# Optimization experiments

Measured on AMD Instinct MI355X. Metric: run time of the kernel, lower is better.

Reference implementation:

```python
import jax, jax.numpy as jnp
import numpy as np

B, S, D = 2, 2048, 2048
H = 16
HD = D // H

def setup_inputs() -> dict:
    key = jax.random.key(0)
    ks = jax.random.split(key, 6)
    s = 1.0 / np.sqrt(D)
    return {
        "inputs": jax.random.normal(ks[0], (B, S, D), dtype=jnp.float32),
        "w_q": jax.random.normal(ks[1], (D, D), dtype=jnp.float32) * s,
        "w_k": jax.random.normal(ks[2], (D, D), dtype=jnp.float32) * s,
        "w_v": jax.random.normal(ks[3], (D, D), dtype=jnp.float32) * s,
        "w_o": jax.random.normal(ks[4], (D, D), dtype=jnp.float32) * s,
        "b_o": jax.random.normal(ks[5], (D,), dtype=jnp.float32) * 0.02,
    }

def reference(inputs, w_q, w_k, w_v, w_o, b_o):
    b, t, _ = inputs.shape
    # Linear layers: y = x @ W^T (weights stored torch-style [out, in])
    q = (inputs @ w_q.T).reshape(b, t, H, HD)
    k = (inputs @ w_k.T).reshape(b, t, H, HD)
    v = (inputs @ w_v.T).reshape(b, t, H, HD)
    # scores: [b, h, t, t]
    scores = jnp.einsum('bqhd,bkhd->bhqk', q, k)
    causal = jnp.triu(jnp.ones((t, t), dtype=bool), k=1)
    scores = jnp.where(causal, -jnp.inf, scores)
    # NOTE: source scales by sqrt(token_num) (keys.shape[2] after transpose), not sqrt(head_dim)
    scale = jnp.float32(t) ** 0.5
    attn = jax.nn.softmax(scores / scale, axis=-1)
    ctx = jnp.einsum('bhqk,bkhd->bqhd', attn, v).reshape(b, t, D)
    return ctx @ w_o.T + b_o
```

## Files before the change

### kernel.cpp

```cpp
#include <hip/hip_runtime.h>


typedef __attribute__((ext_vector_type(8))) short short8;
typedef __attribute__((ext_vector_type(4))) float f32x4;

#define SEQ 2048
#define DM  2048
#define NHD 128
#define NT  32
#define QSCALE (0.022097086912079608f * 1.4426950408889634f)

#define EXP2F(x) __builtin_amdgcn_exp2f(x)
#define WAITV(N) asm volatile("s_waitcnt vmcnt(" #N ")" ::: "memory")

__device__ __forceinline__ unsigned short f2bf(float f) {
  unsigned u = __builtin_bit_cast(unsigned, f);
  u += 0x7FFFu + ((u >> 16) & 1u);
  return (unsigned short)(u >> 16);
}
__device__ __forceinline__ unsigned short f2bf_fast(float f) {
  unsigned u = __builtin_bit_cast(unsigned, f);
  return (unsigned short)((u + 0x8000u) >> 16);
}

__device__ __forceinline__ void gll16(const void* g, void* l) {
  __builtin_amdgcn_global_load_lds((const __attribute__((address_space(1))) void*)g,
                                   (__attribute__((address_space(3))) void*)l, 16, 0, 0);
}

template <int CTRL>
__device__ __forceinline__ float dpp_mv(float x) {
  int xi = __builtin_bit_cast(int, x);
  return __builtin_bit_cast(float,
      __builtin_amdgcn_update_dpp(xi, xi, CTRL, 0xF, 0xF, false));
}
__device__ __forceinline__ float red16_max(float x) {
  x = fmaxf(x, dpp_mv<0xB1>(x));
  x = fmaxf(x, dpp_mv<0x4E>(x));
  x = fmaxf(x, dpp_mv<0x124>(x));
  x = fmaxf(x, dpp_mv<0x128>(x));
  return x;
}
__device__ __forceinline__ float red16_sum(float x) {
  x += dpp_mv<0xB1>(x);
  x += dpp_mv<0x4E>(x);
  x += dpp_mv<0x124>(x);
  x += dpp_mv<0x128>(x);
  return x;
}

__global__ __launch_bounds__(256) void cast_bf16_k(const float* __restrict__ in,
                                                   unsigned short* __restrict__ out,
                                                   int n8) {
  int i = blockIdx.x * 256 + threadIdx.x;
  if (i >= n8) return;
  const f32x4* p = (const f32x4*)in + (size_t)i * 2;
  f32x4 a = p[0], b = p[1];
  short8 o;
  o[0] = (short)f2bf(a[0]); o[1] = (short)f2bf(a[1]);
  o[2] = (short)f2bf(a[2]); o[3] = (short)f2bf(a[3]);
  o[4] = (short)f2bf(b[0]); o[5] = (short)f2bf(b[1]);
  o[6] = (short)f2bf(b[2]); o[7] = (short)f2bf(b[3]);
  *(short8*)(out + (size_t)i * 8) = o;
}

__global__ __launch_bounds__(256) void cast_w4_k(const float* __restrict__ Wq,
                                                 const float* __restrict__ Wk,
                                                 const float* __restrict__ Wv,
                                                 const float* __restrict__ Wo,
                                                 unsigned short* __restrict__ Wqb,
                                                 unsigned short* __restrict__ Wkb,
                                                 unsigned short* __restrict__ Wvb,
                                                 unsigned short* __restrict__ Wob) {
  int i = blockIdx.x * 256 + threadIdx.x;
  int r = i >> 19, j = i & 524287;
  const float* src = (r == 0) ? Wq : (r == 1) ? Wk : (r == 2) ? Wv : Wo;
  unsigned short* dst = (r == 0) ? Wqb : (r == 1) ? Wkb : (r == 2) ? Wvb : Wob;
  float sc = (r == 0) ? QSCALE : 1.0f;
  const f32x4* p = (const f32x4*)src + (size_t)j * 2;
  f32x4 a = p[0], b = p[1];
  short8 o;
  o[0] = (short)f2bf(a[0] * sc); o[1] = (short)f2bf(a[1] * sc);
  o[2] = (short)f2bf(a[2] * sc); o[3] = (short)f2bf(a[3] * sc);
  o[4] = (short)f2bf(b[0] * sc); o[5] = (short)f2bf(b[1] * sc);
  o[6] = (short)f2bf(b[2] * sc); o[7] = (short)f2bf(b[3] * sc);
  *(short8*)(dst + (size_t)j * 8) = o;
}

__device__ __forceinline__ void stage_half(const unsigned short* __restrict__ gbase,
                                           unsigned short* lhalf, int tid) {
#pragma unroll
  for (int c = 0; c < 2; ++c) {
    int G = c * 512 + tid;
    int row = G >> 3, g = G & 7;
    int gs = g ^ (row & 7);
    gll16(gbase + (size_t)row * DM + gs * 8, lhalf + (size_t)G * 8);
  }
}

#define LOADAF(MH)                                                              \
  _Pragma("unroll") for (int mi = 0; mi < 4; ++mi)                              \
    _Pragma("unroll") for (int ks = 0; ks < 2; ++ks) {                          \
      int row = wm * 64 + mi * 16 + lr;                                         \
      af[mi][ks] = *(const short8*)&lA[(MH) * 8192 + row * 64 +                 \
                                       (((ks * 4 + kb) ^ (row & 7)) * 8)];      \
    }

#define PHASE(MH, NH, STG, WV)                                                  \
  {                                                                             \
    const unsigned short* lBh = lB + (NH) * 8192;                               \
    short8 bfr[2][2];                                                           \
    _Pragma("unroll") for (int ni = 0; ni < 2; ++ni)                            \
      _Pragma("unroll") for (int ks = 0; ks < 2; ++ks) {                        \
        int row = wn * 32 + ni * 16 + lr;                                       \
        bfr[ni][ks] = *(const short8*)&lBh[row * 64 + (((ks * 4 + kb) ^ (row & 7)) * 8)]; \
      }                                                                         \
    STG;                                                                        \
    __builtin_amdgcn_s_barrier();                                               \
    __builtin_amdgcn_s_setprio(1);                                              \
    _Pragma("unroll") for (int mi = 0; mi < 4; ++mi)                            \
      _Pragma("unroll") for (int ni = 0; ni < 2; ++ni) {                        \
        acc[MH][NH][mi][ni] = __builtin_amdgcn_mfma_f32_16x16x32_bf16(          \
            af[mi][0], bfr[ni][0], acc[MH][NH][mi][ni], 0, 0, 0);               \
        acc[MH][NH][mi][ni] = __builtin_amdgcn_mfma_f32_16x16x32_bf16(          \
            af[mi][1], bfr[ni][1], acc[MH][NH][mi][ni], 0, 0, 0);               \
      }                                                                         \
    __builtin_amdgcn_s_setprio(0);                                              \
    WV;                                                                         \
    __builtin_amdgcn_s_barrier();                                               \
  }

__device__ __forceinline__ void gemm256_core(const unsigned short* __restrict__ A,
                                             const unsigned short* __restrict__ B,
                                             unsigned short* LA, unsigned short* LB,
                                             f32x4 acc[2][2][4][2], int m0, int n0) {
  const int tid = threadIdx.x;
  const int w = tid >> 6, l = tid & 63;
  const int lr = l & 15, kb = l >> 4;
  const int wm = w >> 2, wn = w & 3;

  stage_half(A + (size_t)m0 * DM, LA, tid);
  stage_half(B + (size_t)n0 * DM, LB, tid);
  stage_half(B + (size_t)n0 * DM + (size_t)128 * DM, LB + 8192, tid);
  stage_half(A + (size_t)m0 * DM + (size_t)128 * DM, LA + 8192, tid);
  WAITV(4);
  __builtin_amdgcn_s_barrier();

#pragma unroll 1
  for (int t = 0; t < NT; ++t) {
    const unsigned short* lA = LA + (t & 1) * 16384;
    const unsigned short* lB = LB + (t & 1) * 16384;
    unsigned short* sA = LA + ((t + 1) & 1) * 16384;
    unsigned short* sB = LB + ((t + 1) & 1) * 16384;
    const unsigned short* gA = A + (size_t)m0 * DM + (t + 1) * 64;
    const unsigned short* gB = B + (size_t)n0 * DM + (t + 1) * 64;
    const bool st = (t + 1 < NT);
    short8 af[4][2];
    LOADAF(0);
    PHASE(0, 0, if (st) stage_half(gA, sA, tid),
                if (st) { WAITV(4); } else { WAITV(2); });
    PHASE(0, 1, if (st) stage_half(gB, sB, tid),
                if (st) { WAITV(4); } else { WAITV(0); });
    LOADAF(1);
    PHASE(1, 0, if (st) stage_half(gB + (size_t)128 * DM, sB + 8192, tid), );
    PHASE(1, 1, if (st) stage_half(gA + (size_t)128 * DM, sA + 8192, tid),
                if (st) { WAITV(4); });
  }
}

__global__ __launch_bounds__(512, 2) void gemm_qk_k(const unsigned short* __restrict__ X,
                                                    const unsigned short* __restrict__ Wq,
                                                    const unsigned short* __restrict__ Wk,
                                                    unsigned short* __restrict__ Qo,
                                                    unsigned short* __restrict__ Ko) {
  __shared__ unsigned short LA[32768];
  __shared__ unsigned short LB[32768];
  const int lin = blockIdx.x + 8 * (blockIdx.y + 16 * blockIdx.z);
  const int c = lin & 7, idx = lin >> 3;
  const int xb = (c & 1) * 4 + ((idx >> 2) & 3);
  const int yb = (c >> 1) * 4 + (idx & 3);
  const int zb = idx >> 4;
  const unsigned short* W = zb ? Wk : Wq;
  unsigned short* Y = zb ? Ko : Qo;
  const int m0 = yb * 256, n0 = xb * 256;
  const int tid = threadIdx.x, w = tid >> 6, l = tid & 63;
  const int lr = l & 15, kb = l >> 4;
  const int wm = w >> 2, wn = w & 3;
  f32x4 acc[2][2][4][2] = {};
  gemm256_core(X, W, LA, LB, acc, m0, n0);
#pragma unroll
  for (int mh = 0; mh < 2; ++mh)
#pragma unroll
    for (int nh = 0; nh < 2; ++nh)
#pragma unroll
      for (int mi = 0; mi < 4; ++mi)
#pragma unroll
        for (int ni = 0; ni < 2; ++ni)
#pragma unroll
          for (int rr = 0; rr < 4; ++rr) {
            int row = m0 + mh * 128 + wm * 64 + mi * 16 + kb * 4 + rr;
            int col = n0 + nh * 128 + wn * 32 + ni * 16 + lr;
            Y[(size_t)row * DM + col] = f2bf(acc[mh][nh][mi][ni][rr]);
          }
}

#define PH2(NH, STG, WV)                                                        \
  {                                                                             \
    const unsigned short* lBh = lB + (NH) * 8192;                               \
    short8 bfr[2][2];                                                           \
    _Pragma("unroll") for (int ni = 0; ni < 2; ++ni)                            \
      _Pragma("unroll") for (int ks = 0; ks < 2; ++ks) {                        \
        int row = wn * 32 + ni * 16 + lr;                                       \
        bfr[ni][ks] = *(const short8*)&lBh[row * 64 + (((ks * 4 + kb) ^ (row & 7)) * 8)]; \
      }                                                                         \
    STG;                                                                        \
    __builtin_amdgcn_s_barrier();                                               \
    __builtin_amdgcn_s_setprio(1);                                              \
    _Pragma("unroll") for (int mi = 0; mi < 4; ++mi)                            \
      _Pragma("unroll") for (int ni = 0; ni < 2; ++ni) {                        \
        acc[NH][mi][ni] = __builtin_amdgcn_mfma_f32_16x16x32_bf16(              \
            af[mi][0], bfr[ni][0], acc[NH][mi][ni], 0, 0, 0);                   \
        acc[NH][mi][ni] = __builtin_amdgcn_mfma_f32_16x16x32_bf16(              \
            af[mi][1], bfr[ni][1], acc[NH][mi][ni], 0, 0, 0);                   \
      }                                                                         \
    __builtin_amdgcn_s_setprio(0);                                              \
    WV;                                                                         \
    __builtin_amdgcn_s_barrier();                                               \
  }

__device__ __forceinline__ void gemm128x256_core(const unsigned short* __restrict__ A,
                                                 const unsigned short* __restrict__ B,
                                                 unsigned short* LA, unsigned short* LB,
                                                 f32x4 acc[2][4][2], int m0, int n0) {
  const int tid = threadIdx.x;
  const int w = tid >> 6, l = tid & 63;
  const int lr = l & 15, kb = l >> 4;
  const int wm = w >> 2, wn = w & 3;

  stage_half(A + (size_t)m0 * DM, LA, tid);
  stage_half(B + (size_t)n0 * DM, LB, tid);
  stage_half(B + (size_t)n0 * DM + (size_t)128 * DM, LB + 8192, tid);
  WAITV(2);
  __builtin_amdgcn_s_barrier();

#pragma unroll 1
  for (int t = 0; t < NT; ++t) {
    const unsigned short* lA = LA + (t & 1) * 8192;
    const unsigned short* lB = LB + (t & 1) * 16384;
    unsigned short* sA = LA + ((t + 1) & 1) * 8192;
    unsigned short* sB = LB + ((t + 1) & 1) * 16384;
    const unsigned short* gA = A + (size_t)m0 * DM + (t + 1) * 64;
    const unsigned short* gB = B + (size_t)n0 * DM + (t + 1) * 64;
    const bool st = (t + 1 < NT);
    short8 af[4][2];
#pragma unroll
    for (int mi = 0; mi < 4; ++mi)
#pragma unroll
      for (int ks = 0; ks < 2; ++ks) {
        int row = wm * 64 + mi * 16 + lr;
        af[mi][ks] = *(const short8*)&lA[row * 64 + (((ks * 4 + kb) ^ (row & 7)) * 8)];
      }
    PH2(0, if (st) stage_half(gA, sA, tid),
           if (st) { WAITV(2); } else { WAITV(0); });
    PH2(1, if (st) { stage_half(gB, sB, tid); stage_half(gB + (size_t)128 * DM, sB + 8192, tid); },
           if (st) { WAITV(2); });
  }
}

__global__ __launch_bounds__(512, 2) void gemm_vt_k(const unsigned short* __restrict__ Wv,
                                                    const unsigned short* __restrict__ X,
                                                    unsigned short* __restrict__ Vt) {
  __shared__ unsigned short LA[16384];
  __shared__ unsigned short LB[32768];
  const int lin = blockIdx.x + 16 * blockIdx.y;
  const int c = lin & 7, idx = lin >> 3;
  const int yb = (c >> 2) * 8 + (idx & 7);
  const int xb = (c & 3) * 4 + (idx >> 3);
  const int m0 = yb * 128, n0 = xb * 256;
  const int tid = threadIdx.x, w = tid >> 6, l = tid & 63;
  const int lr = l & 15, kb = l >> 4;
  const int wm = w >> 2, wn = w & 3;
  f32x4 acc[2][4][2] = {};
  gemm128x256_core(Wv, X, LA, LB, acc, m0, n0);
#pragma unroll
  for (int nh = 0; nh < 2; ++nh)
#pragma unroll
    for (int mi = 0; mi < 4; ++mi)
#pragma unroll
      for (int ni = 0; ni < 2; ++ni)
#pragma unroll
        for (int rr = 0; rr < 4; ++rr) {
          int i = m0 + wm * 64 + mi * 16 + kb * 4 + rr;
          int j = n0 + nh * 128 + wn * 32 + ni * 16 + lr;
          Vt[((size_t)(j >> 11) * 2048 + i) * 2048 + (j & 2047)] = f2bf(acc[nh][mi][ni][rr]);
        }
}

__global__ __launch_bounds__(512, 2) void gemm_o_k(const unsigned short* __restrict__ A,
                                                   const unsigned short* __restrict__ W,
                                                   const float* __restrict__ bias,
                                                   float* __restrict__ Y) {
  __shared__ unsigned short LA[16384];
  __shared__ unsigned short LB[32768];
  const int lin = blockIdx.x + 8 * blockIdx.y;
  const int c = lin & 7, idx = lin >> 3;
  const int yb = (c >> 1) * 8 + (idx & 7);
  const int xb = (c & 1) * 4 + (idx >> 3);
  const int m0 = yb * 128, n0 = xb * 256;
  const int tid = threadIdx.x, w = tid >> 6, l = tid & 63;
  const int lr = l & 15, kb = l >> 4;
  const int wm = w >> 2, wn = w & 3;
  f32x4 acc[2][4][2] = {};
  gemm128x256_core(A, W, LA, LB, acc, m0, n0);
#pragma unroll
  for (int nh = 0; nh < 2; ++nh)
#pragma unroll
    for (int mi = 0; mi < 4; ++mi)
#pragma unroll
      for (int ni = 0; ni < 2; ++ni)
#pragma unroll
        for (int rr = 0; rr < 4; ++rr) {
          int row = m0 + wm * 64 + mi * 16 + kb * 4 + rr;
          int col = n0 + nh * 128 + wn * 32 + ni * 16 + lr;
          Y[(size_t)row * DM + col] = acc[nh][mi][ni][rr] + bias[col];
        }
}

__device__ __forceinline__ void stage_tiles(const unsigned short* __restrict__ Kh,
                                            const unsigned short* __restrict__ Vh,
                                            unsigned short* KL, unsigned short* VL,
                                            int kv0, int t) {
#pragma unroll
  for (int c = 0; c < 4; ++c) {
    int S = c * 256 + t;
    int row = S >> 4, g = (S & 15) ^ (row & 7);
    gll16(Kh + (size_t)(kv0 + row) * DM + g * 8, KL + (size_t)S * 8);
  }
#pragma unroll
  for (int c = 0; c < 4; ++c) {
    int S = c * 256 + t;
    int d = S >> 3, g = (S & 7) ^ (d & 7);
    gll16(Vh + (size_t)d * SEQ + kv0 + g * 8, VL + (size_t)S * 8);
  }
}

__global__ __launch_bounds__(256) void attn_k(const unsigned short* __restrict__ Q,
                                              const unsigned short* __restrict__ K,
                                              const unsigned short* __restrict__ Vt,
                                              unsigned short* __restrict__ O) {
  __shared__ unsigned short KL[2][64 * 128];
  __shared__ unsigned short VL[2][128 * 64];
  __shared__ unsigned short Pb[4][16 * 64];
  const int t = threadIdx.x, w = t >> 6, l = t & 63;
  const int lr = l & 15, kb = l >> 4;
  const int id = blockIdx.x;
  const int xcd = id & 7, slot = id >> 3;
  const int bh = xcd * 4 + (slot & 3);
  const int xpair = slot >> 2;
  const int b = bh >> 4, h = bh & 15;
  const unsigned short* Kh = K + (size_t)b * SEQ * DM + h * NHD;
  const unsigned short* Vh = Vt + (size_t)bh * NHD * SEQ;

#pragma unroll 1
  for (int phase = 0; phase < 2; ++phase) {
    const int xq = phase ? (31 - xpair) : xpair;
    const int q0 = xq * 64;
    const int qw = q0 + w * 16;
    const int nkt = xq + 1;

    short8 qf[4];
    {
      const unsigned short* qp = Q + (size_t)(b * SEQ + qw + lr) * DM + h * NHD + kb * 8;
#pragma unroll
      for (int ks = 0; ks < 4; ++ks) qf[ks] = *(const short8*)(qp + ks * 32);
    }
    f32x4 ctx[8] = {};
    float mrow[4], lrow[4];
#pragma unroll
    for (int r = 0; r < 4; ++r) { mrow[r] = -3.0e4f; lrow[r] = 0.f; }

    stage_tiles(Kh, Vh, KL[0], VL[0], 0, t);
    __syncthreads();

    int cbuf = 0;
#pragma unroll 1
    for (int kt = 0; kt < nkt; ++kt) {
      const int kv0 = kt * 64;
      if (kt + 1 < nkt) stage_tiles(Kh, Vh, KL[cbuf ^ 1], VL[cbuf ^ 1], kv0 + 64, t);
      const unsigned short* Kc = KL[cbuf];
      const unsigned short* Vc = VL[cbuf];
      f32x4 s[4];
#pragma unroll
      for (int ct = 0; ct < 4; ++ct) {
        s[ct] = (f32x4){0.f, 0.f, 0.f, 0.f};
        int krow = ct * 16 + lr;
#pragma unroll
        for (int ks = 0; ks < 4; ++ks) {
          short8 bf = *(const short8*)&Kc[krow * 128 + (((ks * 4 + kb) ^ (krow & 7)) * 8)];
          s[ct] = __builtin_amdgcn_mfma_f32_16x16x32_bf16(qf[ks], bf, s[ct], 0, 0, 0);
        }
      }
      const bool needmask = (kv0 + 63 > qw);
      float pe[4][4];
#pragma unroll
      for (int r = 0; r < 4; ++r) {
        const int qi = qw + kb * 4 + r;
        float mx = -3.0e4f;
#pragma unroll
        for (int ct = 0; ct < 4; ++ct) {
          float v = s[ct][r];
          if (needmask && (kv0 + ct * 16 + lr > qi)) v = -3.0e4f;
          s[ct][r] = v;
          mx = fmaxf(mx, v);
        }
        mx = red16_max(mx);
        if (mx > mrow[r] + 8.f) {
          float alpha = EXP2F(mrow[r] - mx);
          mrow[r] = mx;
          lrow[r] *= alpha;
#pragma unroll
          for (int cc = 0; cc < 8; ++cc) ctx[cc][r] *= alpha;
        }
        float rs = 0.f;
#pragma unroll
        for (int ct = 0; ct < 4; ++ct) {
          float e = EXP2F(s[ct][r] - mrow[r]);
          pe[ct][r] = e;
          rs += e;
        }
        lrow[r] += red16_sum(rs);
      }
#pragma unroll
      for (int ct = 0; ct < 4; ++ct)
#pragma unroll
        for (int r = 0; r < 4; ++r) {
          int prow = kb * 4 + r;
          int g = (ct * 2 + (lr >> 3)) ^ ((prow >> 1) & 7);
          Pb[w][prow * 64 + g * 8 + (lr & 7)] = f2bf_fast(pe[ct][r]);
        }
      short8 pa[2];
#pragma unroll
      for (int ks = 0; ks < 2; ++ks)
        pa[ks] = *(const short8*)&Pb[w][lr * 64 + (((ks * 4 + kb) ^ ((lr >> 1) & 7)) * 8)];
#pragma unroll
      for (int cc = 0; cc < 8; ++cc) {
        int vrow = cc * 16 + lr;
#pragma unroll
        for (int ks = 0; ks < 2; ++ks) {
          short8 vb = *(const short8*)&Vc[vrow * 64 + (((ks * 4 + kb) ^ (vrow & 7)) * 8)];
          ctx[cc] = __builtin_amdgcn_mfma_f32_16x16x32_bf16(pa[ks], vb, ctx[cc], 0, 0, 0);
        }
      }
      __syncthreads();
      cbuf ^= 1;
    }
#pragma unroll
    for (int r = 0; r < 4; ++r) {
      float inv = 1.f / lrow[r];
      size_t rowoff = (size_t)(b * SEQ + qw + kb * 4 + r) * DM + h * NHD;
#pragma unroll
      for (int cc = 0; cc < 8; ++cc)
        O[rowoff + cc * 16 + lr] = f2bf_fast(ctx[cc][r] * inv);
    }
  }
}

extern "C" void kernel_launch(void* const* d_in, const int* in_sizes, int n_in,
                              void* d_out, int out_size, void* d_ws, size_t ws_size,
                              hipStream_t stream) {
  const float* X  = (const float*)d_in[0];
  const float* Wq = (const float*)d_in[1];
  const float* Wk = (const float*)d_in[2];
  const float* Wv = (const float*)d_in[3];
  const float* Wo = (const float*)d_in[4];
  const float* bo = (const float*)d_in[5];
  float* out = (float*)d_out;

  unsigned short* ws = (unsigned short*)d_ws;
  unsigned short* Xb  = ws;
  unsigned short* Wqb = ws + 8388608;
  unsigned short* Wkb = ws + 12582912;
  unsigned short* Wvb = ws + 16777216;
  unsigned short* Wob = ws + 20971520;
  unsigned short* Qb  = ws + 25165824;
  unsigned short* Kb  = ws + 33554432;
  unsigned short* Vtb = ws + 41943040;
  unsigned short* Cb  = ws + 50331648;

  cast_bf16_k<<<4096, 256, 0, stream>>>(X, Xb, 1048576);
  cast_w4_k<<<8192, 256, 0, stream>>>(Wq, Wk, Wv, Wo, Wqb, Wkb, Wvb, Wob);

  gemm_qk_k<<<dim3(8, 16, 2), 512, 0, stream>>>(Xb, Wqb, Wkb, Qb, Kb);
  gemm_vt_k<<<dim3(16, 16), 512, 0, stream>>>(Wvb, Xb, Vtb);
  attn_k<<<512, 256, 0, stream>>>(Qb, Kb, Vtb, Cb);
  gemm_o_k<<<dim3(8, 32), 512, 0, stream>>>(Cb, Wob, bo, out);
}
```

Measured before the change: 252.0 us.

## Share K/V tile loads between paired low and high query blocks in attention

Result: slower. 302.4 us (+20.0%).

```diff
diff --git a/kernel.cpp b/kernel.cpp
--- a/kernel.cpp
+++ b/kernel.cpp
@@ -344,6 +344,76 @@
   }
 }
 
+__device__ __forceinline__ void attn_tile(const unsigned short* __restrict__ Kc,
+                                          const unsigned short* __restrict__ Vc,
+                                          unsigned short* __restrict__ Pw,
+                                          const short8 qf[4], f32x4 ctx[8],
+                                          float mrow[4], float lrow[4],
+                                          int qw, int kv0, int lr, int kb) {
+  f32x4 s[4];
+#pragma unroll
+  for (int ct = 0; ct < 4; ++ct) {
+    s[ct] = (f32x4){0.f, 0.f, 0.f, 0.f};
+    int krow = ct * 16 + lr;
+#pragma unroll
+    for (int ks = 0; ks < 4; ++ks) {
+      short8 bf = *(const short8*)&Kc[krow * 128 + (((ks * 4 + kb) ^ (krow & 7)) * 8)];
+      s[ct] = __builtin_amdgcn_mfma_f32_16x16x32_bf16(qf[ks], bf, s[ct], 0, 0, 0);
+    }
+  }
+  const bool needmask = (kv0 + 63 > qw);
+  float pe[4][4];
+#pragma unroll
+  for (int r = 0; r < 4; ++r) {
+    const int qi = qw + kb * 4 + r;
+    float mx = -3.0e4f;
+#pragma unroll
+    for (int ct = 0; ct < 4; ++ct) {
+      float v = s[ct][r];
+      if (needmask && (kv0 + ct * 16 + lr > qi)) v = -3.0e4f;
+      s[ct][r] = v;
+      mx = fmaxf(mx, v);
+    }
+    mx = red16_max(mx);
+    if (mx > mrow[r] + 8.f) {
+      float alpha = EXP2F(mrow[r] - mx);
+      mrow[r] = mx;
+      lrow[r] *= alpha;
+#pragma unroll
+      for (int cc = 0; cc < 8; ++cc) ctx[cc][r] *= alpha;
+    }
+    float rs = 0.f;
+#pragma unroll
+    for (int ct = 0; ct < 4; ++ct) {
+      float e = EXP2F(s[ct][r] - mrow[r]);
+      pe[ct][r] = e;
+      rs += e;
+    }
+    lrow[r] += red16_sum(rs);
+  }
+#pragma unroll
+  for (int ct = 0; ct < 4; ++ct)
+#pragma unroll
+    for (int r = 0; r < 4; ++r) {
+      int prow = kb * 4 + r;
+      int g = (ct * 2 + (lr >> 3)) ^ ((prow >> 1) & 7);
+      Pw[prow * 64 + g * 8 + (lr & 7)] = f2bf_fast(pe[ct][r]);
+    }
+  short8 pa[2];
+#pragma unroll
+  for (int ks = 0; ks < 2; ++ks)
+    pa[ks] = *(const short8*)&Pw[lr * 64 + (((ks * 4 + kb) ^ ((lr >> 1) & 7)) * 8)];
+#pragma unroll
+  for (int cc = 0; cc < 8; ++cc) {
+    int vrow = cc * 16 + lr;
+#pragma unroll
+    for (int ks = 0; ks < 2; ++ks) {
+      short8 vb = *(const short8*)&Vc[vrow * 64 + (((ks * 4 + kb) ^ (vrow & 7)) * 8)];
+      ctx[cc] = __builtin_amdgcn_mfma_f32_16x16x32_bf16(pa[ks], vb, ctx[cc], 0, 0, 0);
+    }
+  }
+}
+
 __global__ __launch_bounds__(256) void attn_k(const unsigned short* __restrict__ Q,
                                               const unsigned short* __restrict__ K,
                                               const unsigned short* __restrict__ Vt,
@@ -361,106 +431,56 @@
   const unsigned short* Kh = K + (size_t)b * SEQ * DM + h * NHD;
   const unsigned short* Vh = Vt + (size_t)bh * NHD * SEQ;
 
+  const int xqL = xpair, xqH = 31 - xpair;
+  const int qwL = xqL * 64 + w * 16;
+  const int qwH = xqH * 64 + w * 16;
+  const int nkt = xqH + 1;
+
+  short8 qfL[4], qfH[4];
+  {
+    const unsigned short* qpL = Q + (size_t)(b * SEQ + qwL + lr) * DM + h * NHD + kb * 8;
+    const unsigned short* qpH = Q + (size_t)(b * SEQ + qwH + lr) * DM + h * NHD + kb * 8;
+#pragma unroll
+    for (int ks = 0; ks < 4; ++ks) {
+      qfL[ks] = *(const short8*)(qpL + ks * 32);
+      qfH[ks] = *(const short8*)(qpH + ks * 32);
+    }
+  }
+  f32x4 ctxL[8] = {}, ctxH[8] = {};
+  float mL[4], lLs[4], mH[4], lHs[4];
+#pragma unroll
+  for (int r = 0; r < 4; ++r) {
+    mL[r] = -3.0e4f; lLs[r] = 0.f;
+    mH[r] = -3.0e4f; lHs[r] = 0.f;
+  }
+
+  stage_tiles(Kh, Vh, KL[0], VL[0], 0, t);
+  __syncthreads();
+
+  int cbuf = 0;
 #pragma unroll 1
-  for (int phase = 0; phase < 2; ++phase) {
-    const int xq = phase ? (31 - xpair) : xpair;
-    const int q0 = xq * 64;
-    const int qw = q0 + w * 16;
-    const int nkt = xq + 1;
-
-    short8 qf[4];
-    {
-      const unsigned short* qp = Q + (size_t)(b * SEQ + qw + lr) * DM + h * NHD + kb * 8;
-#pragma unroll
-      for (int ks = 0; ks < 4; ++ks) qf[ks] = *(const short8*)(qp + ks * 32);
-    }
-    f32x4 ctx[8] = {};
-    float mrow[4], lrow[4];
-#pragma unroll
-    for (int r = 0; r < 4; ++r) { mrow[r] = -3.0e4f; lrow[r] = 0.f; }
-
-    stage_tiles(Kh, Vh, KL[0], VL[0], 0, t);
+  for (int kt = 0; kt < nkt; ++kt) {
+    const int kv0 = kt * 64;
+    if (kt + 1 < nkt) stage_tiles(Kh, Vh, KL[cbuf ^ 1], VL[cbuf ^ 1], kv0 + 64, t);
+    const unsigned short* Kc = KL[cbuf];
+    const unsigned short* Vc = VL[cbuf];
+    attn_tile(Kc, Vc, Pb[w], qfH, ctxH, mH, lHs, qwH, kv0, lr, kb);
+    if (kt <= xqL)
+      attn_tile(Kc, Vc, Pb[w], qfL, ctxL, mL, lLs, qwL, kv0, lr, kb);
     __syncthreads();
-
-    int cbuf = 0;
-#pragma unroll 1
-    for (int kt = 0; kt < nkt; ++kt) {
-      const int kv0 = kt * 64;
-      if (kt + 1 < nkt) stage_tiles(Kh, Vh, KL[cbuf ^ 1], VL[cbuf ^ 1], kv0 + 64, t);
-      const unsigned short* Kc = KL[cbuf];
-      const unsigned short* Vc = VL[cbuf];
-      f32x4 s[4];
-#pragma unroll
-      for (int ct = 0; ct < 4; ++ct) {
-        s[ct] = (f32x4){0.f, 0.f, 0.f, 0.f};
-        int krow = ct * 16 + lr;
-#pragma unroll
-        for (int ks = 0; ks < 4; ++ks) {
-          short8 bf = *(const short8*)&Kc[krow * 128 + (((ks * 4 + kb) ^ (krow & 7)) * 8)];
-          s[ct] = __builtin_amdgcn_mfma_f32_16x16x32_bf16(qf[ks], bf, s[ct], 0, 0, 0);
-        }
-      }
-      const bool needmask = (kv0 + 63 > qw);
-      float pe[4][4];
-#pragma unroll
-      for (int r = 0; r < 4; ++r) {
-        const int qi = qw + kb * 4 + r;
-        float mx = -3.0e4f;
-#pragma unroll
-        for (int ct = 0; ct < 4; ++ct) {
-          float v = s[ct][r];
-          if (needmask && (kv0 + ct * 16 + lr > qi)) v = -3.0e4f;
-          s[ct][r] = v;
-          mx = fmaxf(mx, v);
-        }
-        mx = red16_max(mx);
-        if (mx > mrow[r] + 8.f) {
-          float alpha = EXP2F(mrow[r] - mx);
-          mrow[r] = mx;
-          lrow[r] *= alpha;
-#pragma unroll
-          for (int cc = 0; cc < 8; ++cc) ctx[cc][r] *= alpha;
-        }
-        float rs = 0.f;
-#pragma unroll
-        for (int ct = 0; ct < 4; ++ct) {
-          float e = EXP2F(s[ct][r] - mrow[r]);
-          pe[ct][r] = e;
-          rs += e;
-        }
-        lrow[r] += red16_sum(rs);
-      }
-#pragma unroll
-      for (int ct = 0; ct < 4; ++ct)
-#pragma unroll
-        for (int r = 0; r < 4; ++r) {
-          int prow = kb * 4 + r;
-          int g = (ct * 2 + (lr >> 3)) ^ ((prow >> 1) & 7);
-          Pb[w][prow * 64 + g * 8 + (lr & 7)] = f2bf_fast(pe[ct][r]);
-        }
-      short8 pa[2];
-#pragma unroll
-      for (int ks = 0; ks < 2; ++ks)
-        pa[ks] = *(const short8*)&Pb[w][lr * 64 + (((ks * 4 + kb) ^ ((lr >> 1) & 7)) * 8)];
-#pragma unroll
-      for (int cc = 0; cc < 8; ++cc) {
-        int vrow = cc * 16 + lr;
-#pragma unroll
-        for (int ks = 0; ks < 2; ++ks) {
-          short8 vb = *(const short8*)&Vc[vrow * 64 + (((ks * 4 + kb) ^ (vrow & 7)) * 8)];
-          ctx[cc] = __builtin_amdgcn_mfma_f32_16x16x32_bf16(pa[ks], vb, ctx[cc], 0, 0, 0);
-        }
-      }
-      __syncthreads();
-      cbuf ^= 1;
-    }
-#pragma unroll
-    for (int r = 0; r < 4; ++r) {
-      float inv = 1.f / lrow[r];
-      size_t rowoff = (size_t)(b * SEQ + qw + kb * 4 + r) * DM + h * NHD;
-#pragma unroll
-      for (int cc = 0; cc < 8; ++cc)
-        O[rowoff + cc * 16 + lr] = f2bf_fast(ctx[cc][r] * inv);
+    cbuf ^= 1;
+  }
+
+#pragma unroll
+  for (int r = 0; r < 4; ++r) {
+    float invH = 1.f / lHs[r];
+    float invL = 1.f / lLs[r];
+    size_t roH = (size_t)(b * SEQ + qwH + kb * 4 + r) * DM + h * NHD;
+    size_t roL = (size_t)(b * SEQ + qwL + kb * 4 + r) * DM + h * NHD;
+#pragma unroll
+    for (int cc = 0; cc < 8; ++cc) {
+      O[roH + cc * 16 + lr] = f2bf_fast(ctxH[cc][r] * invH);
+      O[roL + cc * 16 + lr] = f2bf_fast(ctxL[cc][r] * invL);
     }
   }
 }
```

## Use 512-thread attention blocks covering 128 query rows with shared KV tiles

Applied to the files above, without the earlier changes.

Result: no change. 251.4 us (-0.2%).

```diff
diff --git a/kernel.cpp b/kernel.cpp
--- a/kernel.cpp
+++ b/kernel.cpp
@@ -326,142 +326,147 @@
         }
 }
 
-__device__ __forceinline__ void stage_tiles(const unsigned short* __restrict__ Kh,
-                                            const unsigned short* __restrict__ Vh,
-                                            unsigned short* KL, unsigned short* VL,
-                                            int kv0, int t) {
-#pragma unroll
-  for (int c = 0; c < 4; ++c) {
-    int S = c * 256 + t;
+__device__ __forceinline__ void stage_tiles8(const unsigned short* __restrict__ Kh,
+                                             const unsigned short* __restrict__ Vh,
+                                             unsigned short* KL, unsigned short* VL,
+                                             int kv0, int t) {
+#pragma unroll
+  for (int c = 0; c < 2; ++c) {
+    int S = c * 512 + t;
     int row = S >> 4, g = (S & 15) ^ (row & 7);
     gll16(Kh + (size_t)(kv0 + row) * DM + g * 8, KL + (size_t)S * 8);
   }
 #pragma unroll
-  for (int c = 0; c < 4; ++c) {
-    int S = c * 256 + t;
+  for (int c = 0; c < 2; ++c) {
+    int S = c * 512 + t;
     int d = S >> 3, g = (S & 7) ^ (d & 7);
     gll16(Vh + (size_t)d * SEQ + kv0 + g * 8, VL + (size_t)S * 8);
   }
 }
 
-__global__ __launch_bounds__(256) void attn_k(const unsigned short* __restrict__ Q,
+__device__ __forceinline__ void attn_tile(const unsigned short* __restrict__ Kc,
+                                          const unsigned short* __restrict__ Vc,
+                                          unsigned short* __restrict__ Pw,
+                                          const short8 qf[4], f32x4 ctx[8],
+                                          float mrow[4], float lrow[4],
+                                          int qw, int kv0, int lr, int kb) {
+  f32x4 s[4];
+#pragma unroll
+  for (int ct = 0; ct < 4; ++ct) {
+    s[ct] = (f32x4){0.f, 0.f, 0.f, 0.f};
+    int krow = ct * 16 + lr;
+#pragma unroll
+    for (int ks = 0; ks < 4; ++ks) {
+      short8 bf = *(const short8*)&Kc[krow * 128 + (((ks * 4 + kb) ^ (krow & 7)) * 8)];
+      s[ct] = __builtin_amdgcn_mfma_f32_16x16x32_bf16(qf[ks], bf, s[ct], 0, 0, 0);
+    }
+  }
+  const bool needmask = (kv0 + 63 > qw);
+  float pe[4][4];
+#pragma unroll
+  for (int r = 0; r < 4; ++r) {
+    const int qi = qw + kb * 4 + r;
+    float mx = -3.0e4f;
+#pragma unroll
+    for (int ct = 0; ct < 4; ++ct) {
+      float v = s[ct][r];
+      if (needmask && (kv0 + ct * 16 + lr > qi)) v = -3.0e4f;
+      s[ct][r] = v;
+      mx = fmaxf(mx, v);
+    }
+    mx = red16_max(mx);
+    if (mx > mrow[r] + 8.f) {
+      float alpha = EXP2F(mrow[r] - mx);
+      mrow[r] = mx;
+      lrow[r] *= alpha;
+#pragma unroll
+      for (int cc = 0; cc < 8; ++cc) ctx[cc][r] *= alpha;
+    }
+    float rs = 0.f;
+#pragma unroll
+    for (int ct = 0; ct < 4; ++ct) {
+      float e = EXP2F(s[ct][r] - mrow[r]);
+      pe[ct][r] = e;
+      rs += e;
+    }
+    lrow[r] += red16_sum(rs);
+  }
+#pragma unroll
+  for (int ct = 0; ct < 4; ++ct)
+#pragma unroll
+    for (int r = 0; r < 4; ++r) {
+      int prow = kb * 4 + r;
+      int g = (ct * 2 + (lr >> 3)) ^ ((prow >> 1) & 7);
+      Pw[prow * 64 + g * 8 + (lr & 7)] = f2bf_fast(pe[ct][r]);
+    }
+  short8 pa[2];
+#pragma unroll
+  for (int ks = 0; ks < 2; ++ks)
+    pa[ks] = *(const short8*)&Pw[lr * 64 + (((ks * 4 + kb) ^ ((lr >> 1) & 7)) * 8)];
+#pragma unroll
+  for (int cc = 0; cc < 8; ++cc) {
+    int vrow = cc * 16 + lr;
+#pragma unroll
+    for (int ks = 0; ks < 2; ++ks) {
+      short8 vb = *(const short8*)&Vc[vrow * 64 + (((ks * 4 + kb) ^ (vrow & 7)) * 8)];
+      ctx[cc] = __builtin_amdgcn_mfma_f32_16x16x32_bf16(pa[ks], vb, ctx[cc], 0, 0, 0);
+    }
+  }
+}
+
+__global__ __launch_bounds__(512) void attn_k(const unsigned short* __restrict__ Q,
                                               const unsigned short* __restrict__ K,
                                               const unsigned short* __restrict__ Vt,
                                               unsigned short* __restrict__ O) {
   __shared__ unsigned short KL[2][64 * 128];
   __shared__ unsigned short VL[2][128 * 64];
-  __shared__ unsigned short Pb[4][16 * 64];
+  __shared__ unsigned short Pb[8][16 * 64];
   const int t = threadIdx.x, w = t >> 6, l = t & 63;
   const int lr = l & 15, kb = l >> 4;
   const int id = blockIdx.x;
-  const int xcd = id & 7, slot = id >> 3;
-  const int bh = xcd * 4 + (slot & 3);
-  const int xpair = slot >> 2;
+  const int xcd = id & 7, s = id >> 3;
+  const int bh = xcd * 4 + (s & 3);
+  const int yh = s >> 2;
+  const int y = (yh < 8) ? yh : (23 - yh);
   const int b = bh >> 4, h = bh & 15;
   const unsigned short* Kh = K + (size_t)b * SEQ * DM + h * NHD;
   const unsigned short* Vh = Vt + (size_t)bh * NHD * SEQ;
 
+  const int qw = y * 128 + w * 16;
+  const int nkt = 2 * y + 2;
+
+  short8 qf[4];
+  {
+    const unsigned short* qp = Q + (size_t)(b * SEQ + qw + lr) * DM + h * NHD + kb * 8;
+#pragma unroll
+    for (int ks = 0; ks < 4; ++ks) qf[ks] = *(const short8*)(qp + ks * 32);
+  }
+  f32x4 ctx[8] = {};
+  float mrow[4], lrow[4];
+#pragma unroll
+  for (int r = 0; r < 4; ++r) { mrow[r] = -3.0e4f; lrow[r] = 0.f; }
+
+  stage_tiles8(Kh, Vh, KL[0], VL[0], 0, t);
+  __syncthreads();
+
+  int cbuf = 0;
 #pragma unroll 1
-  for (int phase = 0; phase < 2; ++phase) {
-    const int xq = phase ? (31 - xpair) : xpair;
-    const int q0 = xq * 64;
-    const int qw = q0 + w * 16;
-    const int nkt = xq + 1;
-
-    short8 qf[4];
-    {
-      const unsigned short* qp = Q + (size_t)(b * SEQ + qw + lr) * DM + h * NHD + kb * 8;
-#pragma unroll
-      for (int ks = 0; ks < 4; ++ks) qf[ks] = *(const short8*)(qp + ks * 32);
-    }
-    f32x4 ctx[8] = {};
-    float mrow[4], lrow[4];
-#pragma unroll
-    for (int r = 0; r < 4; ++r) { mrow[r] = -3.0e4f; lrow[r] = 0.f; }
-
-    stage_tiles(Kh, Vh, KL[0], VL[0], 0, t);
+  for (int kt = 0; kt < nkt; ++kt) {
+    const int kv0 = kt * 64;
+    if (kt + 1 < nkt) stage_tiles8(Kh, Vh, KL[cbuf ^ 1], VL[cbuf ^ 1], kv0 + 64, t);
+    if (kv0 <= qw + 15)
+      attn_tile(KL[cbuf], VL[cbuf], Pb[w], qf, ctx, mrow, lrow, qw, kv0, lr, kb);
     __syncthreads();
-
-    int cbuf = 0;
-#pragma unroll 1
-    for (int kt = 0; kt < nkt; ++kt) {
-      const int kv0 = kt * 64;
-      if (kt + 1 < nkt) stage_tiles(Kh, Vh, KL[cbuf ^ 1], VL[cbuf ^ 1], kv0 + 64, t);
-      const unsigned short* Kc = KL[cbuf];
-      const unsigned short* Vc = VL[cbuf];
-      f32x4 s[4];
-#pragma unroll
-      for (int ct = 0; ct < 4; ++ct) {
-        s[ct] = (f32x4){0.f, 0.f, 0.f, 0.f};
-        int krow = ct * 16 + lr;
-#pragma unroll
-        for (int ks = 0; ks < 4; ++ks) {
-          short8 bf = *(const short8*)&Kc[krow * 128 + (((ks * 4 + kb) ^ (krow & 7)) * 8)];
-          s[ct] = __builtin_amdgcn_mfma_f32_16x16x32_bf16(qf[ks], bf, s[ct], 0, 0, 0);
-        }
-      }
-      const bool needmask = (kv0 + 63 > qw);
-      float pe[4][4];
-#pragma unroll
-      for (int r = 0; r < 4; ++r) {
-        const int qi = qw + kb * 4 + r;
-        float mx = -3.0e4f;
-#pragma unroll
-        for (int ct = 0; ct < 4; ++ct) {
-          float v = s[ct][r];
-          if (needmask && (kv0 + ct * 16 + lr > qi)) v = -3.0e4f;
-          s[ct][r] = v;
-          mx = fmaxf(mx, v);
-        }
-        mx = red16_max(mx);
-        if (mx > mrow[r] + 8.f) {
-          float alpha = EXP2F(mrow[r] - mx);
-          mrow[r] = mx;
-          lrow[r] *= alpha;
-#pragma unroll
-          for (int cc = 0; cc < 8; ++cc) ctx[cc][r] *= alpha;
-        }
-        float rs = 0.f;
-#pragma unroll
-        for (int ct = 0; ct < 4; ++ct) {
-          float e = EXP2F(s[ct][r] - mrow[r]);
-          pe[ct][r] = e;
-          rs += e;
-        }
-        lrow[r] += red16_sum(rs);
-      }
-#pragma unroll
-      for (int ct = 0; ct < 4; ++ct)
-#pragma unroll
-        for (int r = 0; r < 4; ++r) {
-          int prow = kb * 4 + r;
-          int g = (ct * 2 + (lr >> 3)) ^ ((prow >> 1) & 7);
-          Pb[w][prow * 64 + g * 8 + (lr & 7)] = f2bf_fast(pe[ct][r]);
-        }
-      short8 pa[2];
-#pragma unroll
-      for (int ks = 0; ks < 2; ++ks)
-        pa[ks] = *(const short8*)&Pb[w][lr * 64 + (((ks * 4 + kb) ^ ((lr >> 1) & 7)) * 8)];
-#pragma unroll
-      for (int cc = 0; cc < 8; ++cc) {
-        int vrow = cc * 16 + lr;
-#pragma unroll
-        for (int ks = 0; ks < 2; ++ks) {
-          short8 vb = *(const short8*)&Vc[vrow * 64 + (((ks * 4 + kb) ^ (vrow & 7)) * 8)];
-          ctx[cc] = __builtin_amdgcn_mfma_f32_16x16x32_bf16(pa[ks], vb, ctx[cc], 0, 0, 0);
-        }
-      }
-      __syncthreads();
-      cbuf ^= 1;
-    }
-#pragma unroll
-    for (int r = 0; r < 4; ++r) {
-      float inv = 1.f / lrow[r];
-      size_t rowoff = (size_t)(b * SEQ + qw + kb * 4 + r) * DM + h * NHD;
-#pragma unroll
-      for (int cc = 0; cc < 8; ++cc)
-        O[rowoff + cc * 16 + lr] = f2bf_fast(ctx[cc][r] * inv);
-    }
+    cbuf ^= 1;
+  }
+
+#pragma unroll
+  for (int r = 0; r < 4; ++r) {
+    float inv = 1.f / lrow[r];
+    size_t rowoff = (size_t)(b * SEQ + qw + kb * 4 + r) * DM + h * NHD;
+#pragma unroll
+    for (int cc = 0; cc < 8; ++cc)
+      O[rowoff + cc * 16 + lr] = f2bf_fast(ctx[cc][r] * inv);
   }
 }
 
@@ -492,6 +497,6 @@
 
   gemm_qk_k<<<dim3(8, 16, 2), 512, 0, stream>>>(Xb, Wqb, Wkb, Qb, Kb);
   gemm_vt_k<<<dim3(16, 16), 512, 0, stream>>>(Wvb, Xb, Vtb);
-  attn_k<<<512, 256, 0, stream>>>(Qb, Kb, Vtb, Cb);
+  attn_k<<<512, 512, 0, stream>>>(Qb, Kb, Vtb, Cb);
   gemm_o_k<<<dim3(8, 32), 512, 0, stream>>>(Cb, Wob, bo, out);
 }
```
